# Kernel optimization log

Hardware: AMD Instinct MI355X
Metric: run time of the kernel (lower is better)

## Reference

```python
import jax, jax.numpy as jnp
import numpy as np

H = 32          # num_heads
D = 64          # head_dim
HID = 2048      # hidden_size
THETA = 10000.0
GATE_NORM = 16.0
EPS = 1e-6


def rope_interleaved(x):
    # x: [B, T, H, D]; interleaved RoPE over full head_dim, 'fla' inv_freq
    B, T, nh, d = x.shape
    inv_freq = 1.0 / (THETA ** (jnp.arange(0, d, 2, dtype=jnp.float32) / d))  # [d/2]
    t = jnp.arange(T, dtype=jnp.float32)
    freqs = t[:, None] * inv_freq[None, :]                 # [T, d/2]
    cos = jnp.cos(freqs)[None, :, None, :]                 # [1,T,1,d/2]
    sin = jnp.sin(freqs)[None, :, None, :]
    x1 = x[..., 0::2]
    x2 = x[..., 1::2]
    r1 = x1 * cos - x2 * sin
    r2 = x1 * sin + x2 * cos
    out = jnp.stack([r1, r2], axis=-1).reshape(x.shape)    # re-interleave pairs
    return out


def setup_inputs() -> dict:
    key = jax.random.key(0)
    ks = jax.random.split(key, 7)
    s = HID ** -0.5
    return {
        "hidden_states": jax.random.normal(ks[0], (1, 2048, HID), dtype=jnp.float32),
        "Wq": jax.random.normal(ks[1], (HID, HID), dtype=jnp.float32) * s,
        "Wk": jax.random.normal(ks[2], (HID, HID), dtype=jnp.float32) * s,
        "Wv": jax.random.normal(ks[3], (HID, HID), dtype=jnp.float32) * s,
        "Wg": jax.random.normal(ks[4], (HID, HID), dtype=jnp.float32) * s,
        "Wgk": jax.random.normal(ks[5], (H, HID), dtype=jnp.float32) * s,
        "Wo": jax.random.normal(ks[6], (HID, HID), dtype=jnp.float32) * s,
    }


def reference(hidden_states, Wq, Wk, Wv, Wg, Wgk, Wo):
    B, T, _ = hidden_states.shape
    q = (hidden_states @ Wq.T).reshape(B, T, H, D)
    k = (hidden_states @ Wk.T).reshape(B, T, H, D)
    v = (hidden_states @ Wv.T).reshape(B, T, H, D)
    g = hidden_states @ Wg.T                                   # [B,T,HID]
    gk = jax.nn.log_sigmoid(hidden_states @ Wgk.T) / GATE_NORM  # [B,T,H], <= 0

    q = rope_interleaved(q)
    k = rope_interleaved(k)

    # gated retention (simple GLA) in parallel form:
    # o_t = scale * sum_{s<=t} exp(G_t - G_s) (q_t . k_s) v_s,  G = cumsum(gk)
    scale = D ** -0.5
    G = jnp.cumsum(gk, axis=1)                                 # [B,T,H]
    Gt = jnp.transpose(G, (0, 2, 1))                           # [B,H,T]
    decay = Gt[:, :, :, None] - Gt[:, :, None, :]              # [B,H,T,T] (<=0 on causal part)
    causal = jnp.tril(jnp.ones((T, T), dtype=bool))
    scores = jnp.einsum('bihd,bjhd->bhij', q, k) * scale
    A = jnp.where(causal[None, None], jnp.exp(decay) * scores, 0.0)
    o = jnp.einsum('bhij,bjhd->bihd', A, v)                    # [B,T,H,D]

    # FusedRMSNormGated (no affine): rmsnorm(o) * silu(gate)
    var = jnp.mean(jnp.square(o), axis=-1, keepdims=True)
    o = o * jax.lax.rsqrt(var + EPS)
    gate = g.reshape(B, T, H, D)
    o = o * jax.nn.silu(gate)

    o = o.reshape(B, T, HID) @ Wo.T
    return o
```

## Files before the change

### kernel.cpp

```cpp
#include <hip/hip_runtime.h>
#include <hip/hip_bf16.h>
#include <stdint.h>

#define TT 2048
#define NH 32
#define HD 64
#define HIDDEN 2048

typedef __attribute__((ext_vector_type(8))) short short8;
typedef __attribute__((ext_vector_type(4))) short short4v;
typedef __attribute__((ext_vector_type(4))) float f32x4;

__device__ inline short f2bf(float x) {
  __hip_bfloat16 h = __float2bfloat16(x);
  return __builtin_bit_cast(short, h);
}

__device__ inline void gload16(const void* g, void* l) {
  __builtin_amdgcn_global_load_lds(
      (const __attribute__((address_space(1))) unsigned int*)g,
      (__attribute__((address_space(3))) unsigned int*)l, 16, 0, 0);
}

__global__ void cast_bf16(const float* __restrict__ src, short* __restrict__ dst, int n) {
  int idx = blockIdx.x * 256 + threadIdx.x;
  int i = idx * 4;
  if (i < n) {
    float4 v = *reinterpret_cast<const float4*>(src + i);
    short4v o;
    o[0] = f2bf(v.x); o[1] = f2bf(v.y); o[2] = f2bf(v.z); o[3] = f2bf(v.w);
    *reinterpret_cast<short4v*>(dst + i) = o;
  }
}

__global__ void rope_table_kernel(float2* __restrict__ rt) {
  int idx = blockIdx.x * 256 + threadIdx.x;
  int t = idx >> 5, i = idx & 31;
  double inv = pow(10000.0, -(double)i / 32.0);
  float f = (float)t * (float)inv;
  float2 cs; cs.x = cosf(f); cs.y = sinf(f);
  rt[idx] = cs;
}

__global__ __launch_bounds__(256) void gk_kernel(const float* __restrict__ hidden,
                                                 const float* __restrict__ Wgk,
                                                 float* __restrict__ gk) {
  int t = blockIdx.x;
  __shared__ float row[HIDDEN];
  int tid = threadIdx.x;
  const float4* hr = reinterpret_cast<const float4*>(hidden + (size_t)t * HIDDEN);
#pragma unroll
  for (int i = 0; i < 2; i++) {
    float4 v = hr[tid + i * 256];
    *reinterpret_cast<float4*>(&row[(tid + i * 256) * 4]) = v;
  }
  __syncthreads();
  int w = tid >> 6, l = tid & 63;
  for (int hh = 0; hh < 8; hh++) {
    int h = w * 8 + hh;
    const float* wr = Wgk + (size_t)h * HIDDEN;
    float acc = 0.f;
#pragma unroll
    for (int i = 0; i < 32; i++) acc = fmaf(row[i * 64 + l], wr[i * 64 + l], acc);
#pragma unroll
    for (int m = 1; m < 64; m <<= 1) acc += __shfl_xor(acc, m, 64);
    if (l == 0) {
      float x = acc;
      float ls = fminf(x, 0.f) - log1pf(__expf(-fabsf(x)));
      gk[(size_t)h * TT + t] = ls * (1.0f / 16.0f);
    }
  }
}

__global__ void cumsum_kernel(const float* __restrict__ gk, float* __restrict__ G) {
  int h = blockIdx.x;
  int l = threadIdx.x;
  float carry = 0.f;
  for (int c = 0; c < 32; c++) {
    float x = gk[(size_t)h * TT + c * 64 + l];
#pragma unroll
    for (int ofs = 1; ofs < 64; ofs <<= 1) {
      float y = __shfl_up(x, ofs, 64);
      if (l >= ofs) x += y;
    }
    x += carry;
    G[(size_t)h * TT + c * 64 + l] = x;
    carry = __shfl(x, 63, 64);
  }
}

__global__ __launch_bounds__(256) void gemm_bt(const short* __restrict__ A,
                                               const short* __restrict__ B,
                                               float* __restrict__ C,
                                               int M, int N, int K) {
  __shared__ short As[128 * 32];
  __shared__ short Bs[128 * 32];
  int tm = blockIdx.y * 128;
  int tn = blockIdx.x * 128;
  int tid = threadIdx.x;
  int w = tid >> 6, l = tid & 63;
  int wr = w >> 1, wc = w & 1;
  int srow = l >> 2;
  int scol = (l & 3) * 8;
  int lg = l >> 4, lr = l & 15;
  f32x4 acc[4][4] = {};
  for (int k0 = 0; k0 < K; k0 += 32) {
    __syncthreads();
#pragma unroll
    for (int i = 0; i < 2; i++) {
      int r = i * 64 + w * 16 + srow;
      gload16(A + (size_t)(tm + r) * K + k0 + scol, &As[(i * 64 + w * 16) * 32]);
      gload16(B + (size_t)(tn + r) * K + k0 + scol, &Bs[(i * 64 + w * 16) * 32]);
    }
    __syncthreads();
    short8 a[4], b[4];
#pragma unroll
    for (int m = 0; m < 4; m++)
      a[m] = *reinterpret_cast<const short8*>(&As[(wr * 64 + m * 16 + lr) * 32 + lg * 8]);
#pragma unroll
    for (int n = 0; n < 4; n++)
      b[n] = *reinterpret_cast<const short8*>(&Bs[(wc * 64 + n * 16 + lr) * 32 + lg * 8]);
#pragma unroll
    for (int m = 0; m < 4; m++)
#pragma unroll
      for (int n = 0; n < 4; n++)
        acc[m][n] = __builtin_amdgcn_mfma_f32_16x16x32_bf16(a[m], b[n], acc[m][n], 0, 0, 0);
  }
#pragma unroll
  for (int m = 0; m < 4; m++)
#pragma unroll
    for (int n = 0; n < 4; n++)
#pragma unroll
      for (int r = 0; r < 4; r++) {
        int row = tm + wr * 64 + m * 16 + lg * 4 + r;
        int col = tn + wc * 64 + n * 16 + lr;
        C[(size_t)row * N + col] = acc[m][n][r];
      }
}

__global__ __launch_bounds__(256) void rope_post(const float* __restrict__ QKVG,
                                                 const float2* __restrict__ rt,
                                                 short* __restrict__ qb,
                                                 short* __restrict__ kb,
                                                 short* __restrict__ vtb) {
  int tb = blockIdx.x, h = blockIdx.y;
  int tid = threadIdx.x;
  int p = tid & 31;
  int r0 = tid >> 5;
#pragma unroll
  for (int rr = 0; rr < 8; rr++) {
    int rloc = r0 * 8 + rr;
    int t = tb * 64 + rloc;
    float2 cs = rt[(size_t)t * 32 + p];
    float2 xq = *reinterpret_cast<const float2*>(&QKVG[(size_t)t * 8192 + h * 64 + 2 * p]);
    float r1 = xq.x * cs.x - xq.y * cs.y;
    float r2 = xq.x * cs.y + xq.y * cs.x;
    short4v dummy;
    ushort2 uq; uq.x = (unsigned short)f2bf(r1); uq.y = (unsigned short)f2bf(r2);
    *reinterpret_cast<ushort2*>(&qb[((size_t)h * TT + t) * 64 + 2 * p]) = uq;
    float2 xk = *reinterpret_cast<const float2*>(&QKVG[(size_t)t * 8192 + 2048 + h * 64 + 2 * p]);
    r1 = xk.x * cs.x - xk.y * cs.y;
    r2 = xk.x * cs.y + xk.y * cs.x;
    ushort2 uk; uk.x = (unsigned short)f2bf(r1); uk.y = (unsigned short)f2bf(r2);
    *reinterpret_cast<ushort2*>(&kb[((size_t)h * TT + t) * 64 + 2 * p]) = uk;
  }
  __shared__ float vt[64][65];
  int c = tid & 63;
  int rbase = tid >> 6;
#pragma unroll
  for (int k4 = 0; k4 < 16; k4++) {
    int rloc = rbase * 16 + k4;
    vt[rloc][c] = QKVG[(size_t)(tb * 64 + rloc) * 8192 + 4096 + h * 64 + c];
  }
  __syncthreads();
#pragma unroll
  for (int k4 = 0; k4 < 16; k4++) {
    int d = rbase * 16 + k4;
    float val = vt[c][d];
    vtb[((size_t)h * HD + d) * TT + tb * 64 + c] = f2bf(val);
  }
}

__global__ __launch_bounds__(256) void attn_kernel(const short* __restrict__ qbuf,
                                                   const short* __restrict__ kbuf,
                                                   const short* __restrict__ vtbuf,
                                                   const float* __restrict__ G,
                                                   const float* __restrict__ QKVG,
                                                   short* __restrict__ z) {
  int qblk = blockIdx.x, h = blockIdx.y;
  __shared__ short Ks[64 * 64];
  __shared__ short Vs[64 * 64];
  __shared__ short Ps[4][16 * 64];
  int tid = threadIdx.x, w = tid >> 6, l = tid & 63;
  int lg = l >> 4, lr = l & 15;

  int tq_row = qblk * 64 + w * 16 + lr;
  short8 aq0 = *reinterpret_cast<const short8*>(&qbuf[((size_t)h * TT + tq_row) * HD + lg * 8]);
  short8 aq1 = *reinterpret_cast<const short8*>(&qbuf[((size_t)h * TT + tq_row) * HD + 32 + lg * 8]);

  int tq0 = qblk * 64 + w * 16 + lg * 4;
  float Gq[4];
#pragma unroll
  for (int r = 0; r < 4; r++) Gq[r] = G[(size_t)h * TT + tq0 + r];

  f32x4 o[4] = {};
  int sj = w * 8 + (l >> 3);

  for (int jb = 0; jb <= qblk; jb++) {
    __syncthreads();
#pragma unroll
    for (int i = 0; i < 2; i++) {
      int row = i * 32 + sj;
      int cb = ((l & 7) ^ (row & 7)) * 8;
      gload16(&kbuf[((size_t)h * TT + jb * 64 + row) * HD + cb], &Ks[(i * 32 + w * 8) * 64]);
      gload16(&vtbuf[((size_t)h * HD + row) * TT + jb * 64 + cb], &Vs[(i * 32 + w * 8) * 64]);
    }
    __syncthreads();

#pragma unroll
    for (int n = 0; n < 4; n++) {
      int j = n * 16 + lr;
      short8 bk0 = *reinterpret_cast<const short8*>((const char*)Ks + j * 128 + ((lg * 16) ^ ((j & 7) << 4)));
      short8 bk1 = *reinterpret_cast<const short8*>((const char*)Ks + j * 128 + ((64 + lg * 16) ^ ((j & 7) << 4)));
      f32x4 s = {};
      s = __builtin_amdgcn_mfma_f32_16x16x32_bf16(aq0, bk0, s, 0, 0, 0);
      s = __builtin_amdgcn_mfma_f32_16x16x32_bf16(aq1, bk1, s, 0, 0, 0);
      int tj = jb * 64 + n * 16 + lr;
      float Gk = G[(size_t)h * TT + tj];
#pragma unroll
      for (int r = 0; r < 4; r++) {
        int tq = tq0 + r;
        float pv = 0.f;
        if (tj <= tq) pv = __expf(Gq[r] - Gk) * 0.125f * s[r];
        int qloc = lg * 4 + r;
        int jloc = n * 16 + lr;
        int boff = qloc * 128 + ((jloc * 2) ^ ((qloc & 7) << 4));
        *reinterpret_cast<short*>((char*)&Ps[w][0] + boff) = f2bf(pv);
      }
    }

    short8 pa0 = *reinterpret_cast<const short8*>((const char*)&Ps[w][0] + lr * 128 + ((lg * 16) ^ ((lr & 7) << 4)));
    short8 pa1 = *reinterpret_cast<const short8*>((const char*)&Ps[w][0] + lr * 128 + ((64 + lg * 16) ^ ((lr & 7) << 4)));
#pragma unroll
    for (int n = 0; n < 4; n++) {
      int d = n * 16 + lr;
      short8 bv0 = *reinterpret_cast<const short8*>((const char*)Vs + d * 128 + ((lg * 16) ^ ((d & 7) << 4)));
      short8 bv1 = *reinterpret_cast<const short8*>((const char*)Vs + d * 128 + ((64 + lg * 16) ^ ((d & 7) << 4)));
      o[n] = __builtin_amdgcn_mfma_f32_16x16x32_bf16(pa0, bv0, o[n], 0, 0, 0);
      o[n] = __builtin_amdgcn_mfma_f32_16x16x32_bf16(pa1, bv1, o[n], 0, 0, 0);
    }
  }

  float sums[4];
#pragma unroll
  for (int r = 0; r < 4; r++) {
    float ss = 0.f;
#pragma unroll
    for (int n = 0; n < 4; n++) ss += o[n][r] * o[n][r];
#pragma unroll
    for (int m = 1; m < 16; m <<= 1) ss += __shfl_xor(ss, m, 64);
    sums[r] = ss;
  }
#pragma unroll
  for (int r = 0; r < 4; r++) {
    int tq = tq0 + r;
    float rstd = rsqrtf(sums[r] * (1.0f / 64.0f) + 1e-6f);
#pragma unroll
    for (int n = 0; n < 4; n++) {
      int d = n * 16 + lr;
      float gv = QKVG[(size_t)tq * 8192 + 6144 + h * 64 + d];
      float sg = gv / (1.0f + __expf(-gv));
      float val = o[n][r] * rstd * sg;
      z[(size_t)tq * HIDDEN + h * 64 + d] = f2bf(val);
    }
  }
}

extern "C" void kernel_launch(void* const* d_in, const int* in_sizes, int n_in,
                              void* d_out, int out_size, void* d_ws, size_t ws_size,
                              hipStream_t stream) {
  const float* hidden = (const float*)d_in[0];
  const float* Wq = (const float*)d_in[1];
  const float* Wk = (const float*)d_in[2];
  const float* Wv = (const float*)d_in[3];
  const float* Wg = (const float*)d_in[4];
  const float* Wgk = (const float*)d_in[5];
  const float* Wo = (const float*)d_in[6];
  float* out = (float*)d_out;
  char* ws = (char*)d_ws;

  const size_t NELEM = (size_t)TT * HIDDEN;
  short* XbZ  = (short*)(ws + 0);
  short* Wb   = (short*)(ws + 8388608);
  short* Wob  = (short*)(ws + 41943040);
  float* QKVG = (float*)(ws + 50331648);
  short* qbuf = (short*)(ws + 117440512);
  short* kbuf = (short*)(ws + 125829120);
  short* vtbuf= (short*)(ws + 134217728);
  float* gkb  = (float*)(ws + 142606336);
  float* Gb   = (float*)(ws + 142868480);
  float2* rt  = (float2*)(ws + 143130624);

  int nblk = (int)(NELEM / 4 / 256);
  cast_bf16<<<nblk, 256, 0, stream>>>(hidden, XbZ, (int)NELEM);
  cast_bf16<<<nblk, 256, 0, stream>>>(Wq, Wb + 0 * NELEM, (int)NELEM);
  cast_bf16<<<nblk, 256, 0, stream>>>(Wk, Wb + 1 * NELEM, (int)NELEM);
  cast_bf16<<<nblk, 256, 0, stream>>>(Wv, Wb + 2 * NELEM, (int)NELEM);
  cast_bf16<<<nblk, 256, 0, stream>>>(Wg, Wb + 3 * NELEM, (int)NELEM);
  cast_bf16<<<nblk, 256, 0, stream>>>(Wo, Wob, (int)NELEM);
  rope_table_kernel<<<256, 256, 0, stream>>>(rt);
  gk_kernel<<<TT, 256, 0, stream>>>(hidden, Wgk, gkb);
  cumsum_kernel<<<NH, 64, 0, stream>>>(gkb, Gb);
  gemm_bt<<<dim3(64, 16), 256, 0, stream>>>(XbZ, Wb, QKVG, TT, 4 * HIDDEN, HIDDEN);
  rope_post<<<dim3(32, NH), 256, 0, stream>>>(QKVG, rt, qbuf, kbuf, vtbuf);
  attn_kernel<<<dim3(32, NH), 256, 0, stream>>>(qbuf, kbuf, vtbuf, Gb, QKVG, XbZ);
  gemm_bt<<<dim3(16, 16), 256, 0, stream>>>(XbZ, Wob, out, TT, HIDDEN, HIDDEN);
}
```

Baseline: 433.9 us.

## Add 256x256 pipelined QKVG GEMM, fuse weight casts, tweak rope table and priorities

```diff
diff --git a/kernel.cpp b/kernel.cpp
--- a/kernel.cpp
+++ b/kernel.cpp
@@ -22,22 +22,37 @@
       (__attribute__((address_space(3))) unsigned int*)l, 16, 0, 0);
 }
 
-__global__ void cast_bf16(const float* __restrict__ src, short* __restrict__ dst, int n) {
-  int idx = blockIdx.x * 256 + threadIdx.x;
-  int i = idx * 4;
-  if (i < n) {
-    float4 v = *reinterpret_cast<const float4*>(src + i);
-    short4v o;
-    o[0] = f2bf(v.x); o[1] = f2bf(v.y); o[2] = f2bf(v.z); o[3] = f2bf(v.w);
-    *reinterpret_cast<short4v*>(dst + i) = o;
-  }
+__global__ void cast6(const float* __restrict__ s0, const float* __restrict__ s1,
+                      const float* __restrict__ s2, const float* __restrict__ s3,
+                      const float* __restrict__ s4, const float* __restrict__ s5,
+                      short* __restrict__ d0, short* __restrict__ d1,
+                      short* __restrict__ d2, short* __restrict__ d3,
+                      short* __restrict__ d4, short* __restrict__ d5) {
+  int t0 = blockIdx.x * 256 + threadIdx.x;
+  int stride = gridDim.x * 256;
+  const int NG = 1 << 20;
+#define CAST_LOOP(S, D)                                            \
+  for (int g = t0; g < NG; g += stride) {                          \
+    float4 v = *reinterpret_cast<const float4*>(S + (size_t)g * 4);\
+    short4v o;                                                     \
+    o[0] = f2bf(v.x); o[1] = f2bf(v.y);                            \
+    o[2] = f2bf(v.z); o[3] = f2bf(v.w);                            \
+    *reinterpret_cast<short4v*>(D + (size_t)g * 4) = o;            \
+  }
+  CAST_LOOP(s0, d0)
+  CAST_LOOP(s1, d1)
+  CAST_LOOP(s2, d2)
+  CAST_LOOP(s3, d3)
+  CAST_LOOP(s4, d4)
+  CAST_LOOP(s5, d5)
+#undef CAST_LOOP
 }
 
 __global__ void rope_table_kernel(float2* __restrict__ rt) {
   int idx = blockIdx.x * 256 + threadIdx.x;
   int t = idx >> 5, i = idx & 31;
-  double inv = pow(10000.0, -(double)i / 32.0);
-  float f = (float)t * (float)inv;
+  float inv = exp2f(-(float)i * (13.287712379549449f / 32.0f));
+  float f = (float)t * inv;
   float2 cs; cs.x = cosf(f); cs.y = sinf(f);
   rt[idx] = cs;
 }
@@ -87,6 +102,115 @@
     G[(size_t)h * TT + c * 64 + l] = x;
     carry = __shfl(x, 63, 64);
   }
+}
+
+__global__ __launch_bounds__(512, 1) void gemm256(const short* __restrict__ A,
+                                                  const short* __restrict__ B,
+                                                  float* __restrict__ C,
+                                                  int M, int N, int K) {
+  __shared__ short lds[4 * 16384];
+  int tid = threadIdx.x;
+  int w = tid >> 6, l = tid & 63;
+  int wr = w >> 2, wc = w & 3;
+  int lr = l & 15, lg = l >> 4;
+
+  int bx = blockIdx.x, by = blockIdx.y;
+  if ((gridDim.x & 7) == 0) {
+    int id = by * gridDim.x + bx;
+    int sx = gridDim.x >> 3;
+    int xcd = id & 7, p = id >> 3;
+    bx = xcd * sx + p % sx;
+    by = p / sx;
+  }
+  size_t tm = (size_t)by * 256, tn = (size_t)bx * 256;
+
+  int srow = l >> 2;
+  int schunk = (((l & 3) ^ ((l >> 2) & 3) ^ ((l >> 4) & 3)) << 3);
+  const short* pA0 = A + (size_t)(tm + w * 16 + srow) * K + schunk;
+  const short* pA1 = A + (size_t)(tm + 128 + w * 16 + srow) * K + schunk;
+  const short* pB0 = B + (size_t)(tn + w * 16 + srow) * K + schunk;
+  const short* pB1 = B + (size_t)(tn + 128 + w * 16 + srow) * K + schunk;
+  int dA0 = (0 * 128 + w * 16) * 32;
+  int dA1 = (1 * 128 + w * 16) * 32;
+  int dB0 = 8192 + (0 * 128 + w * 16) * 32;
+  int dB1 = 8192 + (1 * 128 + w * 16) * 32;
+
+  int rchunk = ((lg ^ ((lr & 3) ^ ((lr >> 2) & 3))) << 3);
+  int baseA = (wr * 128 + lr) * 32 + rchunk;
+  int baseB = (wc * 64 + lr) * 32 + rchunk;
+
+  f32x4 acc[8][4] = {};
+  int nt = K >> 5;
+
+  for (int t = 0; t < 3; ++t) {
+    short* sb = &lds[(t & 3) * 16384];
+    gload16(pA0 + (size_t)t * 32, sb + dA0);
+    gload16(pA1 + (size_t)t * 32, sb + dA1);
+    gload16(pB0 + (size_t)t * 32, sb + dB0);
+    gload16(pB1 + (size_t)t * 32, sb + dB1);
+  }
+  asm volatile("s_waitcnt vmcnt(8)" ::: "memory");
+  __builtin_amdgcn_s_barrier();
+
+  for (int t = 0; t < nt; ++t) {
+    const short* As = &lds[(t & 3) * 16384];
+    const short* Bs = As + 8192;
+    int pf = t + 3;
+    bool do_pf = pf < nt;
+    short* pfb = &lds[(pf & 3) * 16384];
+
+    short8 a[4], b[4];
+#pragma unroll
+    for (int mi = 0; mi < 4; mi++)
+      a[mi] = *reinterpret_cast<const short8*>(As + baseA + mi * 512);
+#pragma unroll
+    for (int ni = 0; ni < 4; ni++)
+      b[ni] = *reinterpret_cast<const short8*>(Bs + baseB + ni * 512);
+    if (do_pf) {
+      gload16(pA0 + (size_t)pf * 32, pfb + dA0);
+      gload16(pA1 + (size_t)pf * 32, pfb + dA1);
+    }
+    __builtin_amdgcn_s_barrier();
+    asm volatile("s_waitcnt lgkmcnt(0)" ::: "memory");
+    __builtin_amdgcn_s_setprio(1);
+#pragma unroll
+    for (int mi = 0; mi < 4; mi++)
+#pragma unroll
+      for (int ni = 0; ni < 4; ni++)
+        acc[mi][ni] = __builtin_amdgcn_mfma_f32_16x16x32_bf16(a[mi], b[ni], acc[mi][ni], 0, 0, 0);
+    __builtin_amdgcn_s_setprio(0);
+    __builtin_amdgcn_s_barrier();
+
+#pragma unroll
+    for (int mi = 0; mi < 4; mi++)
+      a[mi] = *reinterpret_cast<const short8*>(As + baseA + (mi + 4) * 512);
+    if (do_pf) {
+      gload16(pB0 + (size_t)pf * 32, pfb + dB0);
+      gload16(pB1 + (size_t)pf * 32, pfb + dB1);
+    }
+    __builtin_amdgcn_s_barrier();
+    asm volatile("s_waitcnt lgkmcnt(0)" ::: "memory");
+    __builtin_amdgcn_s_setprio(1);
+#pragma unroll
+    for (int mi = 0; mi < 4; mi++)
+#pragma unroll
+      for (int ni = 0; ni < 4; ni++)
+        acc[mi + 4][ni] = __builtin_amdgcn_mfma_f32_16x16x32_bf16(a[mi], b[ni], acc[mi + 4][ni], 0, 0, 0);
+    __builtin_amdgcn_s_setprio(0);
+    asm volatile("s_waitcnt vmcnt(8)" ::: "memory");
+    __builtin_amdgcn_s_barrier();
+  }
+
+#pragma unroll
+  for (int mi = 0; mi < 8; mi++)
+#pragma unroll
+    for (int ni = 0; ni < 4; ni++)
+#pragma unroll
+      for (int r = 0; r < 4; r++) {
+        size_t row = tm + wr * 128 + mi * 16 + lg * 4 + r;
+        size_t col = tn + wc * 64 + ni * 16 + lr;
+        C[row * N + col] = acc[mi][ni][r];
+      }
 }
 
 __global__ __launch_bounds__(256) void gemm_bt(const short* __restrict__ A,
@@ -155,7 +279,6 @@
     float2 xq = *reinterpret_cast<const float2*>(&QKVG[(size_t)t * 8192 + h * 64 + 2 * p]);
     float r1 = xq.x * cs.x - xq.y * cs.y;
     float r2 = xq.x * cs.y + xq.y * cs.x;
-    short4v dummy;
     ushort2 uq; uq.x = (unsigned short)f2bf(r1); uq.y = (unsigned short)f2bf(r2);
     *reinterpret_cast<ushort2*>(&qb[((size_t)h * TT + t) * 64 + 2 * p]) = uq;
     float2 xk = *reinterpret_cast<const float2*>(&QKVG[(size_t)t * 8192 + 2048 + h * 64 + 2 * p]);
@@ -241,6 +364,7 @@
 
     short8 pa0 = *reinterpret_cast<const short8*>((const char*)&Ps[w][0] + lr * 128 + ((lg * 16) ^ ((lr & 7) << 4)));
     short8 pa1 = *reinterpret_cast<const short8*>((const char*)&Ps[w][0] + lr * 128 + ((64 + lg * 16) ^ ((lr & 7) << 4)));
+    __builtin_amdgcn_s_setprio(1);
 #pragma unroll
     for (int n = 0; n < 4; n++) {
       int d = n * 16 + lr;
@@ -249,6 +373,7 @@
       o[n] = __builtin_amdgcn_mfma_f32_16x16x32_bf16(pa0, bv0, o[n], 0, 0, 0);
       o[n] = __builtin_amdgcn_mfma_f32_16x16x32_bf16(pa1, bv1, o[n], 0, 0, 0);
     }
+    __builtin_amdgcn_s_setprio(0);
   }
 
   float sums[4];
@@ -301,17 +426,13 @@
   float* Gb   = (float*)(ws + 142868480);
   float2* rt  = (float2*)(ws + 143130624);
 
-  int nblk = (int)(NELEM / 4 / 256);
-  cast_bf16<<<nblk, 256, 0, stream>>>(hidden, XbZ, (int)NELEM);
-  cast_bf16<<<nblk, 256, 0, stream>>>(Wq, Wb + 0 * NELEM, (int)NELEM);
-  cast_bf16<<<nblk, 256, 0, stream>>>(Wk, Wb + 1 * NELEM, (int)NELEM);
-  cast_bf16<<<nblk, 256, 0, stream>>>(Wv, Wb + 2 * NELEM, (int)NELEM);
-  cast_bf16<<<nblk, 256, 0, stream>>>(Wg, Wb + 3 * NELEM, (int)NELEM);
-  cast_bf16<<<nblk, 256, 0, stream>>>(Wo, Wob, (int)NELEM);
+  cast6<<<2048, 256, 0, stream>>>(hidden, Wq, Wk, Wv, Wg, Wo,
+                                  XbZ, Wb + 0 * NELEM, Wb + 1 * NELEM,
+                                  Wb + 2 * NELEM, Wb + 3 * NELEM, Wob);
   rope_table_kernel<<<256, 256, 0, stream>>>(rt);
   gk_kernel<<<TT, 256, 0, stream>>>(hidden, Wgk, gkb);
   cumsum_kernel<<<NH, 64, 0, stream>>>(gkb, Gb);
-  gemm_bt<<<dim3(64, 16), 256, 0, stream>>>(XbZ, Wb, QKVG, TT, 4 * HIDDEN, HIDDEN);
+  gemm256<<<dim3(32, 8), 512, 0, stream>>>(XbZ, Wb, QKVG, TT, 4 * HIDDEN, HIDDEN);
   rope_post<<<dim3(32, NH), 256, 0, stream>>>(QKVG, rt, qbuf, kbuf, vtbuf);
   attn_kernel<<<dim3(32, NH), 256, 0, stream>>>(qbuf, kbuf, vtbuf, Gb, QKVG, XbZ);
   gemm_bt<<<dim3(16, 16), 256, 0, stream>>>(XbZ, Wob, out, TT, HIDDEN, HIDDEN);
```

New measurement: 394.5 us. -9.1%, faster.
